# Performance work log

Measured on AMD Instinct MI355X. Metric: run time of the kernel, lower is better.

Reference implementation:

```python
import jax, jax.numpy as jnp
import numpy as np

N, T = 64, 256
V, E, K = 32000, 256, 128


def setup_inputs() -> dict:
    key = jax.random.key(0)
    ks = jax.random.split(key, 7)
    x = jax.random.randint(ks[0], (N, T), 0, V)
    embed_w = jax.random.normal(ks[1], (V, E), dtype=jnp.float32) * 0.02
    # nn.Linear(embed_dim, K*K, bias=False), weight.uniform_(-1, 1)
    trans_w = jax.random.uniform(ks[2], (K * K, E), dtype=jnp.float32, minval=-1.0, maxval=1.0)
    # nn.Linear(1, K): weight [K,1], bias [K]
    start_w = jax.random.normal(ks[3], (K, 1), dtype=jnp.float32)
    start_b = jax.random.normal(ks[4], (K,), dtype=jnp.float32) * 0.1
    # nn.Embedding(K, K) cluster embeddings
    emb_cluster_w = jax.random.normal(ks[5], (K, K), dtype=jnp.float32)
    # nn.Linear(K, vocab, bias=False), weight.uniform_(-1, 1) -> weight [V, K]
    emit_w = jax.random.uniform(ks[6], (V, K), dtype=jnp.float32, minval=-1.0, maxval=1.0)
    return {"x": x, "embed_w": embed_w, "trans_w": trans_w, "start_w": start_w,
            "start_b": start_b, "emb_cluster_w": emb_cluster_w, "emit_w": emit_w}


def reference(x, embed_w, trans_w, start_w, start_b, emb_cluster_w, emit_w):
    n, t = x.shape
    k = emb_cluster_w.shape[0]
    ex = embed_w[x]                                            # [N,T,E]
    # Emissions: log_softmax(emit(emb_cluster(i))) per cluster -> [K,V]
    log_emit = jax.nn.log_softmax(emb_cluster_w @ emit_w.T, axis=-1)
    log_emit_t = log_emit.T                                    # [V,K]
    # start(dummy): ones[N,1] @ W.T + b = W[:,0]+b, same per row
    pre = jax.nn.log_softmax(start_w[:, 0] + start_b)          # [K]
    pre = jnp.broadcast_to(pre, (n, k))
    xs = (jnp.swapaxes(ex[:, :-1, :], 0, 1),                   # [T-1,N,E]
          x[:, 1:].T)                                          # [T-1,N]
    def step(pre_alpha, inp):
        x_prev, w_t = inp
        tran = jax.nn.log_softmax((x_prev @ trans_w.T).reshape(n, k, k), axis=-1)
        cur = jax.nn.logsumexp(pre_alpha[:, :, None] + tran, axis=1)   # [N,K]
        cur = cur + log_emit_t[w_t]                            # add log p(w_t | state)
        return cur, None
    cur, _ = jax.lax.scan(step, pre, xs)
    return -jnp.mean(jax.nn.logsumexp(cur, axis=1))
```

## Files before the change

### kernel.cpp

```cpp
#include <hip/hip_runtime.h>
#include <cstdint>
#include <cstddef>

#define N_SEQ 64
#define T_LEN 256
#define VOCAB 32000
#define EDIM  256
#define KS    128
#define KK    16384
#define MROWS 16384
#define MREAL 16320
#define GPART 16

typedef short  short8  __attribute__((ext_vector_type(8)));
typedef float  floatx4 __attribute__((ext_vector_type(4)));
typedef int    intx8   __attribute__((ext_vector_type(8)));

#define LGKM_BARRIER() asm volatile("s_waitcnt lgkmcnt(0)\n\ts_barrier" ::: "memory")
#define LGKM_WAIT()    asm volatile("s_waitcnt lgkmcnt(0)" ::: "memory")

static __device__ __forceinline__ unsigned short f2bf(float f) {
  unsigned u = __float_as_uint(f);
  u += 0x7fffu + ((u >> 16) & 1u);
  return (unsigned short)(u >> 16);
}

static __device__ __forceinline__ float fast_rcp(float x) {
#if __has_builtin(__builtin_amdgcn_rcpf)
  return __builtin_amdgcn_rcpf(x);
#else
  return 1.0f / x;
#endif
}

static __device__ __forceinline__ void gl_lds16(const void* gptr, void* lptr) {
  __builtin_amdgcn_global_load_lds(
      (const __attribute__((address_space(1))) void*)gptr,
      (__attribute__((address_space(3))) void*)lptr, 16, 0, 0);
}

__global__ __launch_bounds__(128) void k_prep(const float* sw, const float* sb, float* pre0) {
  __shared__ float vals[KS];
  __shared__ float MM, LS;
  int tid = threadIdx.x;
  float v = sw[tid] + sb[tid];
  vals[tid] = v;
  __syncthreads();
  if (tid == 0) { float m = vals[0]; for (int i = 1; i < KS; ++i) m = fmaxf(m, vals[i]); MM = m; }
  __syncthreads();
  float e = __expf(v - MM);
  vals[tid] = e;
  __syncthreads();
  if (tid == 0) { float s = 0.f; for (int i = 0; i < KS; ++i) s += vals[i]; LS = MM + __logf(s); }
  __syncthreads();
  pre0[tid] = v - LS;
}

__global__ __launch_bounds__(256) void k_transcvt(const float* tw, unsigned short* tb) {
  int idx = blockIdx.x * 256 + threadIdx.x;
  if (idx >= (KK * EDIM) / 4) return;
  int row = idx >> 6, e4 = idx & 63;
  int rowp = ((row & 127) << 7) | (row >> 7);
  int e4s = (e4 & 0x31) | (((((e4 >> 1) & 7) ^ (rowp & 7))) << 1);
  float4 v = *(const float4*)&tw[(size_t)idx * 4];
  unsigned h0 = f2bf(v.x), h1 = f2bf(v.y), h2 = f2bf(v.z), h3 = f2bf(v.w);
  uint2 o; o.x = h0 | (h1 << 16); o.y = h2 | (h3 << 16);
  *(uint2*)&tb[(size_t)rowp * EDIM + e4s * 4] = o;
}

__global__ __launch_bounds__(256) void k_embed(const int* x, const float* ew, unsigned short* exb) {
  int m = blockIdx.x, e = threadIdx.x;
  int t = m >> 6, n = m & 63;
  float v = 0.f;
  if (m < MREAL) { int tok = x[n * T_LEN + t]; v = ew[(size_t)tok * EDIM + e]; }
  int es = (e & 0xC7) | ((((e >> 3) & 7) ^ (m & 7)) << 3);
  exb[(size_t)m * EDIM + es] = f2bf(v);
}

__global__ __launch_bounds__(256) void k_emitlogits(const float* ecl, const float* emw, float* C) {
  int v0 = blockIdx.x * 64, k0 = blockIdx.y * 64;
  int tid = threadIdx.x;
  __shared__ alignas(16) float At[64 * 17];
  __shared__ alignas(16) float Bt[64 * 17];
  int tx = tid & 15, ty = tid >> 4;
  int r = tid >> 2, q = tid & 3;
  float acc[4][4] = {};
  for (int d0 = 0; d0 < KS; d0 += 16) {
    float4 av = *(const float4*)&ecl[(size_t)(k0 + r) * KS + d0 + q * 4];
    float4 bv = *(const float4*)&emw[(size_t)(v0 + r) * KS + d0 + q * 4];
    __syncthreads();
    At[r * 17 + q * 4 + 0] = av.x; At[r * 17 + q * 4 + 1] = av.y;
    At[r * 17 + q * 4 + 2] = av.z; At[r * 17 + q * 4 + 3] = av.w;
    Bt[r * 17 + q * 4 + 0] = bv.x; Bt[r * 17 + q * 4 + 1] = bv.y;
    Bt[r * 17 + q * 4 + 2] = bv.z; Bt[r * 17 + q * 4 + 3] = bv.w;
    __syncthreads();
    #pragma unroll
    for (int dd = 0; dd < 16; ++dd) {
      float a[4], b[4];
      #pragma unroll
      for (int i = 0; i < 4; ++i) a[i] = At[(ty * 4 + i) * 17 + dd];
      #pragma unroll
      for (int i = 0; i < 4; ++i) b[i] = Bt[(tx * 4 + i) * 17 + dd];
      #pragma unroll
      for (int i = 0; i < 4; ++i)
        #pragma unroll
        for (int jj = 0; jj < 4; ++jj) acc[i][jj] += a[i] * b[jj];
    }
  }
  #pragma unroll
  for (int i = 0; i < 4; ++i) {
    float4 o; o.x = acc[i][0]; o.y = acc[i][1]; o.z = acc[i][2]; o.w = acc[i][3];
    *(float4*)&C[(size_t)(k0 + ty * 4 + i) * VOCAB + v0 + tx * 4] = o;
  }
}

__global__ __launch_bounds__(256) void k_lsec(const float* C, float* lseC) {
  int k = blockIdx.x, tid = threadIdx.x;
  __shared__ float sm[4], ss[4];
  const float* row = C + (size_t)k * VOCAB;
  float m = -1e30f;
  for (int v = tid; v < VOCAB; v += 256) m = fmaxf(m, row[v]);
  #pragma unroll
  for (int s = 1; s < 64; s <<= 1) m = fmaxf(m, __shfl_xor(m, s));
  if ((tid & 63) == 0) sm[tid >> 6] = m;
  __syncthreads();
  m = fmaxf(fmaxf(sm[0], sm[1]), fmaxf(sm[2], sm[3]));
  float sum = 0.f;
  for (int v = tid; v < VOCAB; v += 256) sum += __expf(row[v] - m);
  #pragma unroll
  for (int s = 1; s < 64; s <<= 1) sum += __shfl_xor(sum, s);
  if ((tid & 63) == 0) ss[tid >> 6] = sum;
  __syncthreads();
  if (tid == 0) lseC[k] = m + __logf(ss[0] + ss[1] + ss[2] + ss[3]);
}

__global__ __launch_bounds__(128) void k_emis(const int* x, const float* C, const float* lseC,
                                              float* emis, float* emax) {
  int t = blockIdx.x + 1;
  int n = blockIdx.y;
  int k = threadIdx.x;
  __shared__ float red[2];
  int w = x[n * T_LEN + t];
  float v = C[(size_t)k * VOCAB + w] - lseC[k];
  emis[(size_t)((n << 8) + t) * KS + k] = v;
  float m = v;
  #pragma unroll
  for (int s = 1; s < 64; s <<= 1) m = fmaxf(m, __shfl_xor(m, s));
  if ((k & 63) == 0) red[k >> 6] = m;
  __syncthreads();
  if (k == 0) emax[n * T_LEN + t] = fmaxf(red[0], red[1]);
}

__global__ __launch_bounds__(256) void k_comb(const float* srowP, float* srowR, float* wcomb,
                                              const float* emis, const float* emax,
                                              int m_base, int Rcap, int rows) {
  int id = blockIdx.x * 256 + threadIdx.x;
  if (id >= rows * KS) return;
  float s = 0.f;
  #pragma unroll
  for (int g = 0; g < GPART; ++g) s += srowP[(size_t)g * Rcap * KS + id];
  float r = 1.0f / s;
  srowR[(size_t)m_base * KS + id] = r;
  int m = m_base + (id >> 7);
  int t = m >> 6, n = m & 63, k = id & 127;
  float wv = 0.f;
  if (t >= 1) {
    float e  = emis[(size_t)((n << 8) + t) * KS + k];
    float ex = emax[n * T_LEN + t];
    wv = __expf(e - ex) * r * 4096.0f;
  }
  wcomb[(size_t)m_base * KS + id] = wv;
}

static __device__ __forceinline__ void scan_load_S(const unsigned char* Sbase,
                                                   int l15, int kg, intx8 (&sf)[8]) {
  #pragma unroll
  for (int q = 0; q < 8; ++q) {
    const uint4* p = (const uint4*)(Sbase + (size_t)(q * 16 + l15) * 128 + kg * 32);
    uint4 a = p[0], b = p[1];
    sf[q][0] = a.x; sf[q][1] = a.y; sf[q][2] = a.z; sf[q][3] = a.w;
    sf[q][4] = b.x; sf[q][5] = b.y; sf[q][6] = b.z; sf[q][7] = b.w;
  }
}

static __device__ __forceinline__ void scan_step2(
    int t, int t0, int tLast, int n, int l15, int kg,
    const unsigned char* Sc, const float* wcomb, const float* emax,
    unsigned char* uL8, intx8 (&sf)[8], intx8& uf,
    float (&wv)[8], float& exR, float& M) {
  const float LNS = 8.317766167f;
  floatx4 cz = {0.f, 0.f, 0.f, 0.f};
  float cv[8];
  #pragma unroll
  for (int q = 0; q < 8; ++q) {
    floatx4 d = __builtin_amdgcn_mfma_scale_f32_16x16x128_f8f6f4(
        uf, sf[q], cz, 0, 0, 0, 0x7F7F7F7F, 0, 0x7F7F7F7F);
    cv[q] = d[0];
  }
  int tp = t + 2; if (tp > tLast) tp = tLast;
  scan_load_S(Sc + (size_t)((tp - t0) * 64 + n) * KK, l15, kg, sf);
  float c0 = __uint_as_float(__builtin_amdgcn_readfirstlane(__float_as_uint(cv[0])));
  float rc = fast_rcp(c0);
  #pragma unroll
  for (int q = 0; q < 8; ++q) {
    float up = cv[q] * wv[q] * rc;
    int pk = __builtin_amdgcn_cvt_pk_fp8_f32(up, up, 0, 0);
    uL8[q * 16 + l15] = (unsigned char)(pk & 0xff);
  }
  M += exR + __logf(c0) - LNS;
  #pragma unroll
  for (int q = 0; q < 8; ++q) wv[q] = wcomb[(size_t)(tp * 64 + n) * KS + q * 16 + l15];
  exR = emax[n * T_LEN + tp];
  LGKM_WAIT();
  {
    uint4 ua = *(const uint4*)&uL8[kg * 32];
    uint4 ub = *(const uint4*)&uL8[kg * 32 + 16];
    uf[0] = ua.x; uf[1] = ua.y; uf[2] = ua.z; uf[3] = ua.w;
    uf[4] = ub.x; uf[5] = ub.y; uf[6] = ub.z; uf[7] = ub.w;
  }
}

__global__ __launch_bounds__(256, 2) void k_fused(
    const unsigned short* exb, const unsigned short* trb,
    unsigned char* Sg, float* srowP, int m_base, int Rcap,
    const unsigned char* Ss, const float* srowR, const float* wcomb,
    const float* emis, const float* emax, const float* pre0,
    float* alphaG, float* nll, int t0s, int tcs) {
  __shared__ alignas(16) unsigned short As[128 * 64];
  __shared__ alignas(16) unsigned short Bs[128 * 64];
  __shared__ alignas(16) unsigned char uL8[KS];

  if (blockIdx.x < 64) {
    if (tcs <= 0 || threadIdx.x >= 64) return;
    int n = blockIdx.x;
    int L = threadIdx.x, l15 = L & 15, kg = L >> 4;
    const float SCALE = 4096.0f;
    const float LNS = 8.317766167f;
    int t1 = t0s + tcs, tLast = t1 - 1;
    const float* a0 = (t0s == 1) ? pre0 : (alphaG + (size_t)n * KS);
    float pre[8];
    #pragma unroll
    for (int q = 0; q < 8; ++q) pre[q] = a0[q * 16 + l15];
    float mx = pre[0];
    #pragma unroll
    for (int q = 1; q < 8; ++q) mx = fmaxf(mx, pre[q]);
    #pragma unroll
    for (int s2 = 1; s2 < 16; s2 <<= 1) mx = fmaxf(mx, __shfl_xor(mx, s2));
    float M = mx;
    #pragma unroll
    for (int q = 0; q < 8; ++q) {
      float r0 = srowR[(size_t)((t0s - 1) * 64 + n) * KS + q * 16 + l15];
      float up = __expf(pre[q] - M) * r0 * SCALE;
      int pk = __builtin_amdgcn_cvt_pk_fp8_f32(up, up, 0, 0);
      uL8[q * 16 + l15] = (unsigned char)(pk & 0xff);
    }
    LGKM_WAIT();
    intx8 uf;
    {
      uint4 ua = *(const uint4*)&uL8[kg * 32];
      uint4 ub = *(const uint4*)&uL8[kg * 32 + 16];
      uf[0] = ua.x; uf[1] = ua.y; uf[2] = ua.z; uf[3] = ua.w;
      uf[4] = ub.x; uf[5] = ub.y; uf[6] = ub.z; uf[7] = ub.w;
    }
    intx8 sfA[8], sfB[8];
    scan_load_S(Ss + (size_t)n * KK, l15, kg, sfA);
    int tB = (t0s + 1 < t1) ? (t0s + 1) : tLast;
    scan_load_S(Ss + (size_t)((tB - t0s) * 64 + n) * KK, l15, kg, sfB);
    float wA[8], wB[8];
    #pragma unroll
    for (int q = 0; q < 8; ++q) {
      wA[q] = wcomb[(size_t)(t0s * 64 + n) * KS + q * 16 + l15];
      wB[q] = wcomb[(size_t)(tB * 64 + n) * KS + q * 16 + l15];
    }
    float exA = emax[n * T_LEN + t0s];
    float exB = emax[n * T_LEN + tB];
    int t = t0s;
    while (t < tLast) {
      scan_step2(t, t0s, tLast, n, l15, kg, Ss, wcomb, emax, uL8, sfA, uf, wA, exA, M);
      ++t;
      if (t >= tLast) break;
      scan_step2(t, t0s, tLast, n, l15, kg, Ss, wcomb, emax, uL8, sfB, uf, wB, exB, M);
      ++t;
    }
    {
      floatx4 cz = {0.f, 0.f, 0.f, 0.f};
      float cv[8];
      #pragma unroll
      for (int q = 0; q < 8; ++q) {
        floatx4 d = __builtin_amdgcn_mfma_scale_f32_16x16x128_f8f6f4(
            uf, sfA[q], cz, 0, 0, 0, 0x7F7F7F7F, 0, 0x7F7F7F7F);
        cv[q] = d[0];
      }
      #pragma unroll
      for (int q = 0; q < 8; ++q) {
        float em = emis[(size_t)((n << 8) + tLast) * KS + q * 16 + l15];
        pre[q] = M - LNS + __logf(cv[q]) + em;
      }
    }
    #pragma unroll
    for (int q = 0; q < 8; ++q) alphaG[(size_t)n * KS + q * 16 + l15] = pre[q];
    if (t1 == T_LEN) {
      float m2 = pre[0];
      #pragma unroll
      for (int q = 1; q < 8; ++q) m2 = fmaxf(m2, pre[q]);
      #pragma unroll
      for (int s2 = 1; s2 < 16; s2 <<= 1) m2 = fmaxf(m2, __shfl_xor(m2, s2));
      float e = 0.f;
      #pragma unroll
      for (int q = 0; q < 8; ++q) e += __expf(pre[q] - m2);
      #pragma unroll
      for (int s2 = 1; s2 < 16; s2 <<= 1) e += __shfl_xor(e, s2);
      if (L == 0) nll[n] = m2 + __logf(e);
    }
    return;
  }

  int g = blockIdx.x - 64;
  int bx = g >> 4, grp = g & 15;
  int tid = threadIdx.x, wv = tid >> 6, ln = tid & 63;
  int wc = wv & 1, wm = wv >> 1;
  int m0 = m_base + bx * 128;
  int lr = ln & 15, lk = (ln >> 4) * 8;
  int lg = ln >> 4;
  floatx4 sacc[4][4] = {};
  for (int byi = 0; byi < 8; ++byi) {
    int by = grp * 8 + byi;
    int c0 = by * 128;
    floatx4 acc[4][4] = {};
    for (int k0 = 0; k0 < EDIM; k0 += 64) {
      #pragma unroll
      for (int r = 0; r < 4; ++r) {
        int chunk = (wv * 4 + r) * 64 + ln;
        int row = chunk >> 3, c8 = chunk & 7;
        gl_lds16(&exb[(size_t)(m0 + row) * EDIM + k0 + c8 * 8], &As[(wv * 4 + r) * 512]);
        gl_lds16(&trb[(size_t)(c0 + row) * EDIM + k0 + c8 * 8], &Bs[(wv * 4 + r) * 512]);
      }
      __syncthreads();
      #pragma unroll
      for (int kk = 0; kk < 64; kk += 32) {
        int sw = ((((kk + lk) >> 3) ^ (lr & 7)) << 3);
        short8 af[4], bf[4];
        #pragma unroll
        for (int f = 0; f < 4; ++f)
          af[f] = *(const short8*)&As[(wm * 64 + f * 16 + lr) * 64 + sw];
        #pragma unroll
        for (int f = 0; f < 4; ++f)
          bf[f] = *(const short8*)&Bs[(wc * 64 + f * 16 + lr) * 64 + sw];
        #pragma unroll
        for (int fc = 0; fc < 4; ++fc)
          #pragma unroll
          for (int fm = 0; fm < 4; ++fm)
            acc[fc][fm] = __builtin_amdgcn_mfma_f32_16x16x32_bf16(bf[fc], af[fm], acc[fc][fm], 0, 0, 0);
      }
      LGKM_BARRIER();
    }
    unsigned char* Ts = (unsigned char*)As;
    #pragma unroll
    for (int fc = 0; fc < 4; ++fc) {
      #pragma unroll
      for (int fm = 0; fm < 4; ++fm) {
        floatx4 a = acc[fc][fm];
        float e0 = __expf(a[0]), e1 = __expf(a[1]), e2 = __expf(a[2]), e3 = __expf(a[3]);
        int p = __builtin_amdgcn_cvt_pk_fp8_f32(e0, e1, 0, 0);
        p = __builtin_amdgcn_cvt_pk_fp8_f32(e2, e3, p, 1);
        int mloc = wm * 64 + fm * 16 + lr;
        int cl = wc * 64 + fc * 16 + lg * 4;
        *(int*)&Ts[mloc * 128 + (cl ^ ((mloc & 7) << 4))] = p;
        sacc[fc][fm][0] += e0; sacc[fc][fm][1] += e1;
        sacc[fc][fm][2] += e2; sacc[fc][fm][3] += e3;
      }
    }
    LGKM_BARRIER();
    #pragma unroll
    for (int r = 0; r < 4; ++r) {
      int seg = r * 256 + tid;
      int mloc = seg >> 3, s = seg & 7;
      uint4 v = *(const uint4*)&Ts[mloc * 128 + ((s ^ (mloc & 7)) << 4)];
      *(uint4*)&Sg[(size_t)(bx * 128 + mloc) * KK + c0 + s * 16] = v;
    }
    LGKM_BARRIER();
  }
  #pragma unroll
  for (int fc = 0; fc < 4; ++fc) {
    #pragma unroll
    for (int fm = 0; fm < 4; ++fm) {
      int mloc = bx * 128 + wm * 64 + fm * 16 + lr;
      int i = wc * 64 + fc * 16 + lg * 4;
      *(floatx4*)&srowP[((size_t)grp * Rcap + mloc) * KS + i] = sacc[fc][fm];
    }
  }
}

__global__ __launch_bounds__(64) void k_final(const float* nll, float* out) {
  int tid = threadIdx.x;
  float v = nll[tid];
  #pragma unroll
  for (int s = 1; s < 64; s <<= 1) v += __shfl_xor(v, s);
  if (tid == 0) out[0] = -v / 64.0f;
}

extern "C" void kernel_launch(void* const* d_in, const int* in_sizes, int n_in,
                              void* d_out, int out_size, void* d_ws, size_t ws_size,
                              hipStream_t stream) {
  const int*   x       = (const int*)d_in[0];
  const float* embed_w = (const float*)d_in[1];
  const float* trans_w = (const float*)d_in[2];
  const float* start_w = (const float*)d_in[3];
  const float* start_b = (const float*)d_in[4];
  const float* ecl     = (const float*)d_in[5];
  const float* emw     = (const float*)d_in[6];

  char* w = (char*)d_ws;
  size_t off = 0;
  auto alloc = [&](size_t bytes) -> char* {
    char* p = w + off;
    off = (off + bytes + 255) & ~(size_t)255;
    return p;
  };
  float*          pre0   = (float*)alloc(KS * 4);
  float*          lseC   = (float*)alloc(KS * 4);
  float*          nll    = (float*)alloc(N_SEQ * 4);
  float*          alphaG = (float*)alloc((size_t)N_SEQ * KS * 4);
  float*          emax   = (float*)alloc((size_t)N_SEQ * T_LEN * 4);
  unsigned short* trb    = (unsigned short*)alloc((size_t)KK * EDIM * 2);
  unsigned short* exb    = (unsigned short*)alloc((size_t)MROWS * EDIM * 2);
  float*          emis   = (float*)alloc((size_t)N_SEQ * T_LEN * KS * 4);
  float*          srowR  = (float*)alloc((size_t)MROWS * KS * 4);
  float*          wcomb  = (float*)alloc((size_t)MROWS * KS * 4);
  char* region = w + off;
  size_t avail = (ws_size > off) ? (ws_size - off) : 0;
  float* C = (float*)region;

  int Tc = 2;
  for (int c = 2; c <= 64; c += 2)
    if ((size_t)c * 64 * 40960 <= avail) Tc = c;
  int Rcap = Tc * 64;
  unsigned char* S0    = (unsigned char*)region;
  unsigned char* S1    = (unsigned char*)(region + (size_t)Rcap * KK);
  float*         srowP = (float*)(region + (size_t)2 * Rcap * KK);

  hipLaunchKernelGGL(k_prep,       dim3(1),        dim3(128), 0, stream, start_w, start_b, pre0);
  hipLaunchKernelGGL(k_transcvt,   dim3(4096),     dim3(256), 0, stream, trans_w, trb);
  hipLaunchKernelGGL(k_embed,      dim3(16384),    dim3(256), 0, stream, x, embed_w, exb);
  hipLaunchKernelGGL(k_emitlogits, dim3(500, 2),   dim3(256), 0, stream, ecl, emw, C);
  hipLaunchKernelGGL(k_lsec,       dim3(128),      dim3(256), 0, stream, C, lseC);
  hipLaunchKernelGGL(k_emis,       dim3(255, 64),  dim3(128), 0, stream, x, C, lseC, emis, emax);

  int ct0[140], ctc[140], nc = 0;
  {
    int t0 = 1;
    while (t0 < T_LEN) {
      int tc = T_LEN - t0; if (tc > Tc) tc = Tc;
      ct0[nc] = t0; ctc[nc] = tc; ++nc; t0 += tc;
    }
  }
  for (int c = 0; c <= nc; ++c) {
    bool hasG = (c < nc), hasS = (c > 0);
    int gx = 0, m_base = 0;
    if (hasG) { gx = (ctc[c] * 64 + 127) / 128; m_base = (ct0[c] - 1) * 64; }
    unsigned char* Sg = (c & 1) ? S1 : S0;
    unsigned char* Ssc = ((c - 1) & 1) ? S1 : S0;
    int t0s = hasS ? ct0[c - 1] : 0;
    int tcs = hasS ? ctc[c - 1] : 0;
    hipLaunchKernelGGL(k_fused, dim3(64 + gx * 16), dim3(256), 0, stream,
                       exb, trb, Sg, srowP, m_base, Rcap,
                       Ssc, srowR, wcomb, emis, emax, pre0, alphaG, nll, t0s, tcs);
    if (hasG)
      hipLaunchKernelGGL(k_comb, dim3(gx * 64), dim3(256), 0, stream,
                         srowP, srowR, wcomb, emis, emax, m_base, Rcap, gx * 128);
  }
  hipLaunchKernelGGL(k_final, dim3(1), dim3(64), 0, stream, nll, (float*)d_out);
}
```

Baseline: 576.3 us.

## Split HMM forward scan step across four wavefronts with block barriers

The scan blocks previously ran one 64-lane wavefront that issued 8 MFMAs per time step. The step is now spread over four wavefronts, each computing two 16-column MFMA slices. The normaliser c0 and the new alpha vector are shared through LDS with block-wide barriers, and the final-step emission add is folded into the step function. This cuts the per-step MFMA and load latency on the serial critical path, but adds two s_barrier syncs per time step and extra LDS traffic.

```diff
diff --git a/kernel.cpp b/kernel.cpp
--- a/kernel.cpp
+++ b/kernel.cpp
@@ -18,6 +18,9 @@
 
 #define LGKM_BARRIER() asm volatile("s_waitcnt lgkmcnt(0)\n\ts_barrier" ::: "memory")
 #define LGKM_WAIT()    asm volatile("s_waitcnt lgkmcnt(0)" ::: "memory")
+#define SBAR() do { asm volatile("s_waitcnt lgkmcnt(0)" ::: "memory"); \
+                    __builtin_amdgcn_s_barrier(); \
+                    __builtin_amdgcn_sched_barrier(0); } while (0)
 
 static __device__ __forceinline__ unsigned short f2bf(float f) {
   unsigned u = __float_as_uint(f);
@@ -172,51 +175,57 @@
   wcomb[(size_t)m_base * KS + id] = wv;
 }
 
-static __device__ __forceinline__ void scan_load_S(const unsigned char* Sbase,
-                                                   int l15, int kg, intx8 (&sf)[8]) {
-  #pragma unroll
-  for (int q = 0; q < 8; ++q) {
-    const uint4* p = (const uint4*)(Sbase + (size_t)(q * 16 + l15) * 128 + kg * 32);
-    uint4 a = p[0], b = p[1];
-    sf[q][0] = a.x; sf[q][1] = a.y; sf[q][2] = a.z; sf[q][3] = a.w;
-    sf[q][4] = b.x; sf[q][5] = b.y; sf[q][6] = b.z; sf[q][7] = b.w;
-  }
-}
-
-static __device__ __forceinline__ void scan_step2(
-    int t, int t0, int tLast, int n, int l15, int kg,
-    const unsigned char* Sc, const float* wcomb, const float* emax,
-    unsigned char* uL8, intx8 (&sf)[8], intx8& uf,
-    float (&wv)[8], float& exR, float& M) {
+static __device__ __forceinline__ void load_S2(const unsigned char* Sbase, int j, int kg, intx8& sf) {
+  const uint4* p = (const uint4*)(Sbase + (size_t)j * 128 + kg * 32);
+  uint4 a = p[0], b = p[1];
+  sf[0] = a.x; sf[1] = a.y; sf[2] = a.z; sf[3] = a.w;
+  sf[4] = b.x; sf[5] = b.y; sf[6] = b.z; sf[7] = b.w;
+}
+
+static __device__ __forceinline__ void scan_step4(
+    int i, int L, int t, int t0s, int tLast, int n, int tid, int kg, int j0, int j1,
+    const unsigned char* Ss, const float* wcomb, const float* emis, const float* emax,
+    unsigned char* uL8, float* c0sh,
+    intx8& uf, intx8& s0, intx8& s1, float& w0, float& w1, float& ex,
+    float& M, float& pre_0, float& pre_1) {
   const float LNS = 8.317766167f;
   floatx4 cz = {0.f, 0.f, 0.f, 0.f};
-  float cv[8];
-  #pragma unroll
-  for (int q = 0; q < 8; ++q) {
-    floatx4 d = __builtin_amdgcn_mfma_scale_f32_16x16x128_f8f6f4(
-        uf, sf[q], cz, 0, 0, 0, 0x7F7F7F7F, 0, 0x7F7F7F7F);
-    cv[q] = d[0];
-  }
+  floatx4 d0 = __builtin_amdgcn_mfma_scale_f32_16x16x128_f8f6f4(
+      uf, s0, cz, 0, 0, 0, 0x7F7F7F7F, 0, 0x7F7F7F7F);
+  floatx4 d1 = __builtin_amdgcn_mfma_scale_f32_16x16x128_f8f6f4(
+      uf, s1, cz, 0, 0, 0, 0x7F7F7F7F, 0, 0x7F7F7F7F);
+  float cv0 = d0[0], cv1 = d1[0];
   int tp = t + 2; if (tp > tLast) tp = tLast;
-  scan_load_S(Sc + (size_t)((tp - t0) * 64 + n) * KK, l15, kg, sf);
-  float c0 = __uint_as_float(__builtin_amdgcn_readfirstlane(__float_as_uint(cv[0])));
-  float rc = fast_rcp(c0);
-  #pragma unroll
-  for (int q = 0; q < 8; ++q) {
-    float up = cv[q] * wv[q] * rc;
-    int pk = __builtin_amdgcn_cvt_pk_fp8_f32(up, up, 0, 0);
-    uL8[q * 16 + l15] = (unsigned char)(pk & 0xff);
-  }
-  M += exR + __logf(c0) - LNS;
-  #pragma unroll
-  for (int q = 0; q < 8; ++q) wv[q] = wcomb[(size_t)(tp * 64 + n) * KS + q * 16 + l15];
-  exR = emax[n * T_LEN + tp];
-  LGKM_WAIT();
-  {
+  const unsigned char* Sp = Ss + (size_t)((tp - t0s) * 64 + n) * KK;
+  load_S2(Sp, j0, kg, s0);
+  load_S2(Sp, j1, kg, s1);
+  if (tid == 0) *c0sh = cv0;
+  SBAR();
+  if (i < L - 1) {
+    float c0 = *c0sh;
+    float rc = fast_rcp(c0);
+    float u0 = cv0 * w0 * rc, u1 = cv1 * w1 * rc;
+    int pk0 = __builtin_amdgcn_cvt_pk_fp8_f32(u0, u0, 0, 0);
+    int pk1 = __builtin_amdgcn_cvt_pk_fp8_f32(u1, u1, 0, 0);
+    if (kg == 0) {
+      uL8[j0] = (unsigned char)(pk0 & 0xff);
+      uL8[j1] = (unsigned char)(pk1 & 0xff);
+    }
+    M += ex + __logf(c0) - LNS;
+    w0 = wcomb[(size_t)(tp * 64 + n) * KS + j0];
+    w1 = wcomb[(size_t)(tp * 64 + n) * KS + j1];
+    ex = emax[n * T_LEN + tp];
+    SBAR();
     uint4 ua = *(const uint4*)&uL8[kg * 32];
     uint4 ub = *(const uint4*)&uL8[kg * 32 + 16];
     uf[0] = ua.x; uf[1] = ua.y; uf[2] = ua.z; uf[3] = ua.w;
     uf[4] = ub.x; uf[5] = ub.y; uf[6] = ub.z; uf[7] = ub.w;
+  } else {
+    float em0 = emis[(size_t)((n << 8) + tLast) * KS + j0];
+    float em1 = emis[(size_t)((n << 8) + tLast) * KS + j1];
+    pre_0 = M - LNS + __logf(cv0) + em0;
+    pre_1 = M - LNS + __logf(cv1) + em1;
+    SBAR();
   }
 }
 
@@ -229,32 +238,40 @@
   __shared__ alignas(16) unsigned short As[128 * 64];
   __shared__ alignas(16) unsigned short Bs[128 * 64];
   __shared__ alignas(16) unsigned char uL8[KS];
+  __shared__ float c0sh;
+  __shared__ float redW[4], redE[4];
 
   if (blockIdx.x < 64) {
-    if (tcs <= 0 || threadIdx.x >= 64) return;
+    if (tcs <= 0) return;
     int n = blockIdx.x;
-    int L = threadIdx.x, l15 = L & 15, kg = L >> 4;
+    int tid = threadIdx.x;
+    int w = tid >> 6, ln = tid & 63;
+    int l15 = ln & 15, kg = ln >> 4;
+    int q0 = w * 2;
+    int j0 = q0 * 16 + l15, j1 = j0 + 16;
     const float SCALE = 4096.0f;
-    const float LNS = 8.317766167f;
-    int t1 = t0s + tcs, tLast = t1 - 1;
+    int L = tcs, t1 = t0s + tcs, tLast = t1 - 1;
     const float* a0 = (t0s == 1) ? pre0 : (alphaG + (size_t)n * KS);
-    float pre[8];
+    float pre_0 = a0[j0], pre_1 = a0[j1];
+    float lm = fmaxf(pre_0, pre_1);
     #pragma unroll
-    for (int q = 0; q < 8; ++q) pre[q] = a0[q * 16 + l15];
-    float mx = pre[0];
-    #pragma unroll
-    for (int q = 1; q < 8; ++q) mx = fmaxf(mx, pre[q]);
-    #pragma unroll
-    for (int s2 = 1; s2 < 16; s2 <<= 1) mx = fmaxf(mx, __shfl_xor(mx, s2));
-    float M = mx;
-    #pragma unroll
-    for (int q = 0; q < 8; ++q) {
-      float r0 = srowR[(size_t)((t0s - 1) * 64 + n) * KS + q * 16 + l15];
-      float up = __expf(pre[q] - M) * r0 * SCALE;
-      int pk = __builtin_amdgcn_cvt_pk_fp8_f32(up, up, 0, 0);
-      uL8[q * 16 + l15] = (unsigned char)(pk & 0xff);
-    }
-    LGKM_WAIT();
+    for (int s2 = 1; s2 < 16; s2 <<= 1) lm = fmaxf(lm, __shfl_xor(lm, s2));
+    if (ln == 0) redW[w] = lm;
+    SBAR();
+    float M = fmaxf(fmaxf(redW[0], redW[1]), fmaxf(redW[2], redW[3]));
+    {
+      float r0 = srowR[(size_t)((t0s - 1) * 64 + n) * KS + j0];
+      float r1 = srowR[(size_t)((t0s - 1) * 64 + n) * KS + j1];
+      float u0 = __expf(pre_0 - M) * r0 * SCALE;
+      float u1 = __expf(pre_1 - M) * r1 * SCALE;
+      int pk0 = __builtin_amdgcn_cvt_pk_fp8_f32(u0, u0, 0, 0);
+      int pk1 = __builtin_amdgcn_cvt_pk_fp8_f32(u1, u1, 0, 0);
+      if (kg == 0) {
+        uL8[j0] = (unsigned char)(pk0 & 0xff);
+        uL8[j1] = (unsigned char)(pk1 & 0xff);
+      }
+    }
+    SBAR();
     intx8 uf;
     {
       uint4 ua = *(const uint4*)&uL8[kg * 32];
@@ -262,55 +279,46 @@
       uf[0] = ua.x; uf[1] = ua.y; uf[2] = ua.z; uf[3] = ua.w;
       uf[4] = ub.x; uf[5] = ub.y; uf[6] = ub.z; uf[7] = ub.w;
     }
-    intx8 sfA[8], sfB[8];
-    scan_load_S(Ss + (size_t)n * KK, l15, kg, sfA);
-    int tB = (t0s + 1 < t1) ? (t0s + 1) : tLast;
-    scan_load_S(Ss + (size_t)((tB - t0s) * 64 + n) * KK, l15, kg, sfB);
-    float wA[8], wB[8];
-    #pragma unroll
-    for (int q = 0; q < 8; ++q) {
-      wA[q] = wcomb[(size_t)(t0s * 64 + n) * KS + q * 16 + l15];
-      wB[q] = wcomb[(size_t)(tB * 64 + n) * KS + q * 16 + l15];
-    }
+    intx8 sA0, sA1, sB0, sB1;
+    load_S2(Ss + (size_t)n * KK, j0, kg, sA0);
+    load_S2(Ss + (size_t)n * KK, j1, kg, sA1);
+    int iB = (L > 1) ? 1 : 0;
+    const unsigned char* SpB = Ss + (size_t)(iB * 64 + n) * KK;
+    load_S2(SpB, j0, kg, sB0);
+    load_S2(SpB, j1, kg, sB1);
+    int tB = t0s + iB;
+    float wA0 = wcomb[(size_t)(t0s * 64 + n) * KS + j0];
+    float wA1 = wcomb[(size_t)(t0s * 64 + n) * KS + j1];
+    float wB0 = wcomb[(size_t)(tB * 64 + n) * KS + j0];
+    float wB1 = wcomb[(size_t)(tB * 64 + n) * KS + j1];
     float exA = emax[n * T_LEN + t0s];
     float exB = emax[n * T_LEN + tB];
-    int t = t0s;
-    while (t < tLast) {
-      scan_step2(t, t0s, tLast, n, l15, kg, Ss, wcomb, emax, uL8, sfA, uf, wA, exA, M);
-      ++t;
-      if (t >= tLast) break;
-      scan_step2(t, t0s, tLast, n, l15, kg, Ss, wcomb, emax, uL8, sfB, uf, wB, exB, M);
-      ++t;
-    }
-    {
-      floatx4 cz = {0.f, 0.f, 0.f, 0.f};
-      float cv[8];
-      #pragma unroll
-      for (int q = 0; q < 8; ++q) {
-        floatx4 d = __builtin_amdgcn_mfma_scale_f32_16x16x128_f8f6f4(
-            uf, sfA[q], cz, 0, 0, 0, 0x7F7F7F7F, 0, 0x7F7F7F7F);
-        cv[q] = d[0];
-      }
-      #pragma unroll
-      for (int q = 0; q < 8; ++q) {
-        float em = emis[(size_t)((n << 8) + tLast) * KS + q * 16 + l15];
-        pre[q] = M - LNS + __logf(cv[q]) + em;
-      }
-    }
-    #pragma unroll
-    for (int q = 0; q < 8; ++q) alphaG[(size_t)n * KS + q * 16 + l15] = pre[q];
+    int i = 0, t = t0s;
+    for (;;) {
+      scan_step4(i, L, t, t0s, tLast, n, tid, kg, j0, j1, Ss, wcomb, emis, emax,
+                 uL8, &c0sh, uf, sA0, sA1, wA0, wA1, exA, M, pre_0, pre_1);
+      if (++i >= L) break; ++t;
+      scan_step4(i, L, t, t0s, tLast, n, tid, kg, j0, j1, Ss, wcomb, emis, emax,
+                 uL8, &c0sh, uf, sB0, sB1, wB0, wB1, exB, M, pre_0, pre_1);
+      if (++i >= L) break; ++t;
+    }
+    if (kg == 0) {
+      alphaG[(size_t)n * KS + j0] = pre_0;
+      alphaG[(size_t)n * KS + j1] = pre_1;
+    }
     if (t1 == T_LEN) {
-      float m2 = pre[0];
-      #pragma unroll
-      for (int q = 1; q < 8; ++q) m2 = fmaxf(m2, pre[q]);
+      float m2 = fmaxf(pre_0, pre_1);
       #pragma unroll
       for (int s2 = 1; s2 < 16; s2 <<= 1) m2 = fmaxf(m2, __shfl_xor(m2, s2));
-      float e = 0.f;
-      #pragma unroll
-      for (int q = 0; q < 8; ++q) e += __expf(pre[q] - m2);
-      #pragma unroll
-      for (int s2 = 1; s2 < 16; s2 <<= 1) e += __shfl_xor(e, s2);
-      if (L == 0) nll[n] = m2 + __logf(e);
+      if (ln == 0) redW[w] = m2;
+      SBAR();
+      m2 = fmaxf(fmaxf(redW[0], redW[1]), fmaxf(redW[2], redW[3]));
+      float le = __expf(pre_0 - m2) + __expf(pre_1 - m2);
+      #pragma unroll
+      for (int s2 = 1; s2 < 16; s2 <<= 1) le += __shfl_xor(le, s2);
+      if (ln == 0) redE[w] = le;
+      SBAR();
+      if (tid == 0) nll[n] = m2 + __logf(redE[0] + redE[1] + redE[2] + redE[3]);
     }
     return;
   }
@@ -361,11 +369,11 @@
       for (int fm = 0; fm < 4; ++fm) {
         floatx4 a = acc[fc][fm];
         float e0 = __expf(a[0]), e1 = __expf(a[1]), e2 = __expf(a[2]), e3 = __expf(a[3]);
-        int p = __builtin_amdgcn_cvt_pk_fp8_f32(e0, e1, 0, 0);
-        p = __builtin_amdgcn_cvt_pk_fp8_f32(e2, e3, p, 1);
+        int pq = __builtin_amdgcn_cvt_pk_fp8_f32(e0, e1, 0, 0);
+        pq = __builtin_amdgcn_cvt_pk_fp8_f32(e2, e3, pq, 1);
         int mloc = wm * 64 + fm * 16 + lr;
         int cl = wc * 64 + fc * 16 + lg * 4;
-        *(int*)&Ts[mloc * 128 + (cl ^ ((mloc & 7) << 4))] = p;
+        *(int*)&Ts[mloc * 128 + (cl ^ ((mloc & 7) << 4))] = pq;
         sacc[fc][fm][0] += e0; sacc[fc][fm][1] += e1;
         sacc[fc][fm][2] += e2; sacc[fc][fm][3] += e3;
       }
```

After: 573.3 us. Within noise of the previous version (-0.5%).
